# Optimization experiments

Hardware: AMD Instinct MI355X
Metric: run time of the kernel (lower is better)

## Reference

```python
import jax, jax.numpy as jnp
import numpy as np

B, S, D, H, M = 2, 2048, 1024, 16, 4096  # batch, seqlen, dim, n_heads, max_seq_len
HD = D // H  # head_dim = 64
EPS = 1e-5


def layernorm(x, g, b):
    mu = jnp.mean(x, axis=-1, keepdims=True)
    var = jnp.mean((x - mu) ** 2, axis=-1, keepdims=True)
    return (x - mu) * jax.lax.rsqrt(var + EPS) * g + b


def setup_inputs() -> dict:
    key = jax.random.key(0)
    ks = jax.random.split(key, 5)
    x = jax.random.normal(ks[0], (B, S, D), jnp.float32)
    # causal mask: >=0 -> keep, negative -> drop (forward does att *= mask >= 0)
    i = jnp.arange(S)
    mask = jnp.where(i[None, :] <= i[:, None], 0, -1).astype(jnp.int32)[None, None]
    w1 = jax.random.normal(ks[1], (4 * D, D), jnp.float32) * (D ** -0.5)
    b1 = jnp.zeros((4 * D,), jnp.float32)
    w2 = jax.random.normal(ks[2], (D, D), jnp.float32) * (D ** -0.5)
    b2 = jnp.zeros((D,), jnp.float32)
    g1 = jnp.ones((D,), jnp.float32)
    beta1 = jnp.zeros((D,), jnp.float32)
    g2 = jnp.ones((D,), jnp.float32)
    beta2 = jnp.zeros((D,), jnp.float32)
    pos_w = jax.random.normal(ks[3], (2 * M - 1,), jnp.float32) * 0.02
    return dict(x=x, mask=mask, w1=w1, b1=b1, w2=w2, b2=b2,
                g1=g1, beta1=beta1, g2=g2, beta2=beta2, pos_w=pos_w)


def reference(x, mask, w1, b1, w2, b2, g1, beta1, g2, beta2, pos_w):
    # f1 + silu, split into gate u and q/k/v
    h = jax.nn.silu(x @ w1.T + b1)                      # [B,S,4D]
    u, q, k, v = jnp.split(h, 4, axis=-1)
    to_heads = lambda t: t.reshape(B, S, H, HD).transpose(0, 2, 1, 3)  # [B,H,S,HD]
    u, q, k, v = map(to_heads, (u, q, k, v))
    # relative positional bias: bias[i,j] = pos_w[M-1 + (j - i)]
    rel = jnp.arange(S)[None, :] - jnp.arange(S)[:, None]
    bias = pos_w[M - 1 + rel]                           # [S,S]
    att = jax.nn.silu(jnp.einsum('bhqd,bhkd->bhqk', q, k) + bias)
    att = att * (mask >= 0)                             # [B,H,S,S]
    y = jnp.einsum('bhqk,bhkd->bhqd', att, v) * u
    y = y.transpose(0, 2, 1, 3).reshape(B, S, D)
    y = layernorm(y, g1, beta1)
    y = y @ w2.T + b2
    return layernorm(y + x, g2, beta2)
```

## Files before the change

### kernel.cpp

```cpp
#include <hip/hip_runtime.h>
#include <hip/hip_bf16.h>

#define BN   2
#define SEQ  2048
#define DIM  1024
#define NH   16
#define HD   64
#define D4   4096
#define MAXS 4096

using bf16 = __hip_bfloat16;
typedef __bf16 bf16x8 __attribute__((ext_vector_type(8)));
typedef float  f32x4  __attribute__((ext_vector_type(4)));

__device__ __forceinline__ float bf2f(bf16 v){ return __bfloat162float(v); }
__device__ __forceinline__ bf16  f2bf(float v){ return __float2bfloat16(v); }
__device__ __forceinline__ float silu_f(float v){
  const float e = __expf(-v);
  return v * __builtin_amdgcn_rcpf(1.f + e);
}

__device__ __forceinline__ void async16(void* lds, const void* g){
  __builtin_amdgcn_global_load_lds((const __attribute__((address_space(1))) void*)g,
                                   (__attribute__((address_space(3))) void*)lds, 16, 0, 0);
}
__device__ __forceinline__ f32x4 mfma16(bf16x8 a, bf16x8 b, f32x4 c){
  return __builtin_amdgcn_mfma_f32_16x16x32_bf16(a, b, c, 0, 0, 0);
}

__global__ __launch_bounds__(256) void f2bk3(
    const float* __restrict__ a, bf16* __restrict__ ao, int na,
    const float* __restrict__ b, bf16* __restrict__ bo, int nb,
    const float* __restrict__ c, bf16* __restrict__ co)
{
  int i = (blockIdx.x * 256 + threadIdx.x) * 4;
  const float* in; bf16* out;
  if (i < na){ in = a; out = ao; }
  else if (i < na + nb){ in = b; out = bo; i -= na; }
  else { in = c; out = co; i -= na + nb; }
  const float4 v = *(const float4*)(in + i);
  bf16 t0 = f2bf(v.x), t1 = f2bf(v.y), t2 = f2bf(v.z), t3 = f2bf(v.w);
  ushort4 o;
  o.x = *(unsigned short*)&t0; o.y = *(unsigned short*)&t1;
  o.z = *(unsigned short*)&t2; o.w = *(unsigned short*)&t3;
  *(ushort4*)((unsigned short*)out + i) = o;
}

template<int NTOT>
__global__ __launch_bounds__(256) void gemm_bt(
    const bf16* __restrict__ A, const bf16* __restrict__ W,
    const float* __restrict__ bias, bf16* __restrict__ outb, bf16* __restrict__ vt)
{
  constexpr int K = DIM;
  const int ntiles = NTOT / 128;
  const int m0 = (int)(blockIdx.x / ntiles) * 128;
  const int n0 = (int)(blockIdx.x % ntiles) * 128;
  __shared__ bf16 Al[128*32];
  __shared__ bf16 Bl[128*32];
  const int tid = threadIdx.x, wave = tid>>6, lane = tid&63;
  const int quad = lane>>4, l16 = lane&15;
  const int srow = lane>>2;
  const int sg   = ((lane&3) ^ ((lane>>3)&3)) * 8;
  const int wm = (wave>>1)*64, wn = (wave&1)*64;
  const int rkey = ((l16>>1)&3);

  f32x4 acc[4][4];
  #pragma unroll
  for (int i=0;i<4;i++)
    #pragma unroll
    for (int j=0;j<4;j++) acc[i][j] = (f32x4){0.f,0.f,0.f,0.f};

  const bf16* aB = A + m0*K;
  const bf16* wB = W + n0*K;

  for (int k0 = 0; k0 < K; k0 += 32){
    async16(&Al[wave*1024      ], aB + (wave*32      + srow)*K + k0 + sg);
    async16(&Al[wave*1024 + 512], aB + (wave*32 + 16 + srow)*K + k0 + sg);
    async16(&Bl[wave*1024      ], wB + (wave*32      + srow)*K + k0 + sg);
    async16(&Bl[wave*1024 + 512], wB + (wave*32 + 16 + srow)*K + k0 + sg);
    __syncthreads();
    bf16x8 af[4], bv[4];
    #pragma unroll
    for (int mt=0;mt<4;mt++) af[mt] = *(const bf16x8*)&Al[(wm+mt*16+l16)*32 + (quad ^ rkey)*8];
    #pragma unroll
    for (int nt=0;nt<4;nt++) bv[nt] = *(const bf16x8*)&Bl[(wn+nt*16+l16)*32 + (quad ^ rkey)*8];
    #pragma unroll
    for (int mt=0;mt<4;mt++)
      #pragma unroll
      for (int nt=0;nt<4;nt++)
        acc[mt][nt] = mfma16(af[mt], bv[nt], acc[mt][nt]);
    __syncthreads();
  }

  const bool vtile = (NTOT == 4096) && (n0 >= 3*DIM);
  if (!vtile){
    #pragma unroll
    for (int mt=0;mt<4;mt++){
      #pragma unroll
      for (int nt=0;nt<4;nt++){
        const int row = m0 + wm + mt*16 + quad*4;
        const int col = n0 + wn + nt*16 + l16;
        const float bvv = bias[col];
        #pragma unroll
        for (int r=0;r<4;r++){
          float v = silu_f(acc[mt][nt][r] + bvv);
          outb[(row+r)*NTOT + col] = f2bf(v);
        }
      }
    }
  } else {
    #pragma unroll
    for (int mt=0;mt<4;mt++){
      #pragma unroll
      for (int nt=0;nt<4;nt++){
        const int row = m0 + wm + mt*16 + quad*4;
        const int colg = n0 + wn + nt*16 + l16;
        const float bvv = bias[colg];
        const int col = colg - 3*DIM;
        const int hh = col >> 6, d = col & 63;
        const int bb = row >> 11, sl = row & 2047;
        ushort4 o;
        float v0 = silu_f(acc[mt][nt][0] + bvv);
        float v1 = silu_f(acc[mt][nt][1] + bvv);
        float v2 = silu_f(acc[mt][nt][2] + bvv);
        float v3 = silu_f(acc[mt][nt][3] + bvv);
        bf16 t0=f2bf(v0), t1=f2bf(v1), t2=f2bf(v2), t3=f2bf(v3);
        o.x=*(unsigned short*)&t0; o.y=*(unsigned short*)&t1;
        o.z=*(unsigned short*)&t2; o.w=*(unsigned short*)&t3;
        *(ushort4*)&vt[((bb*NH + hh)*HD + d)*SEQ + sl] = o;
      }
    }
  }
}

__global__ __launch_bounds__(256) void gemm_bt2(
    const bf16* __restrict__ A, const bf16* __restrict__ W,
    const float* __restrict__ bias, const float* __restrict__ resid,
    float* __restrict__ outf)
{
  constexpr int K = DIM, NTOT = DIM;
  const int ntiles = NTOT / 64;
  const int m0 = (int)(blockIdx.x / ntiles) * 128;
  const int n0 = (int)(blockIdx.x % ntiles) * 64;
  __shared__ bf16 Al[128*32];
  __shared__ bf16 Bl[64*32];
  const int tid = threadIdx.x, wave = tid>>6, lane = tid&63;
  const int quad = lane>>4, l16 = lane&15;
  const int srow = lane>>2;
  const int sg   = ((lane&3) ^ ((lane>>3)&3)) * 8;
  const int wm = wave*32;
  const int rkey = ((l16>>1)&3);

  f32x4 acc[2][4];
  #pragma unroll
  for (int i=0;i<2;i++)
    #pragma unroll
    for (int j=0;j<4;j++) acc[i][j] = (f32x4){0.f,0.f,0.f,0.f};

  const bf16* aB = A + m0*K;
  const bf16* wB = W + n0*K;

  for (int k0 = 0; k0 < K; k0 += 32){
    async16(&Al[wave*1024      ], aB + (wave*32      + srow)*K + k0 + sg);
    async16(&Al[wave*1024 + 512], aB + (wave*32 + 16 + srow)*K + k0 + sg);
    async16(&Bl[wave*512       ], wB + (wave*16      + srow)*K + k0 + sg);
    __syncthreads();
    bf16x8 af[2], bv[4];
    #pragma unroll
    for (int mt=0;mt<2;mt++) af[mt] = *(const bf16x8*)&Al[(wm+mt*16+l16)*32 + (quad ^ rkey)*8];
    #pragma unroll
    for (int nt=0;nt<4;nt++) bv[nt] = *(const bf16x8*)&Bl[(nt*16+l16)*32 + (quad ^ rkey)*8];
    #pragma unroll
    for (int mt=0;mt<2;mt++)
      #pragma unroll
      for (int nt=0;nt<4;nt++)
        acc[mt][nt] = mfma16(af[mt], bv[nt], acc[mt][nt]);
    __syncthreads();
  }

  #pragma unroll
  for (int mt=0;mt<2;mt++){
    #pragma unroll
    for (int nt=0;nt<4;nt++){
      const int row = m0 + wm + mt*16 + quad*4;
      const int col = n0 + nt*16 + l16;
      const float bvv = bias[col];
      #pragma unroll
      for (int r=0;r<4;r++){
        outf[(row+r)*NTOT + col] = acc[mt][nt][r] + bvv + resid[(row+r)*NTOT + col];
      }
    }
  }
}

__global__ __launch_bounds__(256) void attn(
    const bf16* __restrict__ h, const bf16* __restrict__ vt,
    const float* __restrict__ pw, bf16* __restrict__ y)
{
  const int bid = blockIdx.x;
  const int g  = (bid & 7) + ((bid >> 7) << 3);
  const int qp = (bid >> 3) & 15;
  const int hh = g & 15, b = g >> 4;
  __shared__ bf16 Kl[128*64];
  __shared__ bf16 Vl[64*128];
  __shared__ bf16 Pl[4][16*136];
  __shared__ float pwl[256];
  const int tid = threadIdx.x, wave = tid>>6, lane = tid&63;
  const int quad = lane>>4, l16 = lane&15;

  const bf16* kgb = h + b*SEQ*D4 + 2*DIM + hh*HD;
  const bf16* vgb = vt + (b*NH + hh)*HD*SEQ;
  const int krow8 = lane>>3;
  const int kgo   = ((lane&7) ^ krow8) * 8;
  const int vrow4 = lane>>4;

  #pragma unroll
  for (int pass = 0; pass < 2; ++pass){
    const int qt = pass ? (31 - qp) : qp;
    const int q0 = qt * 64;

    const bf16* qbase = h + (b*SEQ + q0 + wave*16 + l16)*D4 + DIM + hh*HD;
    bf16x8 qf[2];
    qf[0] = *(const bf16x8*)(qbase + quad*8);
    qf[1] = *(const bf16x8*)(qbase + 32 + quad*8);

    f32x4 oacc[4];
    #pragma unroll
    for (int nt=0;nt<4;nt++) oacc[nt] = (f32x4){0.f,0.f,0.f,0.f};

    const int kmax = q0 + 64;
    for (int k0 = 0; k0 < kmax; k0 += 128){
      #pragma unroll
      for (int t=0;t<4;t++)
        async16(&Kl[(wave*32 + t*8)*64], kgb + (k0 + wave*32 + t*8 + krow8)*D4 + kgo);
      #pragma unroll
      for (int t=0;t<4;t++){
        const int vg = ((lane&15) ^ (t*4 + vrow4)) * 8;
        async16(&Vl[(wave*16 + t*4)*128], vgb + (wave*16 + t*4 + vrow4)*SEQ + k0 + vg);
      }
      const int W0 = MAXS - 1 + k0 - q0 - 63;
      pwl[tid] = pw[W0 + tid];
      __syncthreads();

      f32x4 sacc[8];
      #pragma unroll
      for (int nt=0;nt<8;nt++) sacc[nt] = (f32x4){0.f,0.f,0.f,0.f};
      #pragma unroll
      for (int ks=0;ks<2;ks++){
        #pragma unroll
        for (int nt=0;nt<8;nt++){
          bf16x8 kf = *(const bf16x8*)&Kl[(nt*16 + l16)*64 + ((ks*4 + quad) ^ (l16&7))*8];
          sacc[nt] = mfma16(kf, qf[ks], sacc[nt]);
        }
      }

      const int dq = q0 - k0;
      const int qrl = wave*16 + l16;
      #pragma unroll
      for (int nt=0;nt<8;nt++){
        const int kb = nt*16 + quad*4;
        const int d0 = kb - qrl;
        ushort4 o;
        bf16 tb[4];
        #pragma unroll
        for (int r=0;r<4;r++){
          const int d = kb + r - qrl;
          const float bias = pwl[d + 63];
          const float sv = silu_f(sacc[nt][r] + bias);
          tb[r] = f2bf((d <= dq) ? sv : 0.f);
        }
        (void)d0;
        o.x=*(unsigned short*)&tb[0]; o.y=*(unsigned short*)&tb[1];
        o.z=*(unsigned short*)&tb[2]; o.w=*(unsigned short*)&tb[3];
        *(ushort4*)&Pl[wave][l16*136 + kb] = o;
      }

      #pragma unroll
      for (int ks=0;ks<4;ks++){
        bf16x8 pf = *(const bf16x8*)&Pl[wave][l16*136 + ks*32 + quad*8];
        #pragma unroll
        for (int nt=0;nt<4;nt++){
          bf16x8 vf = *(const bf16x8*)&Vl[(nt*16 + l16)*128 + ((ks*4 + quad) ^ l16)*8];
          oacc[nt] = mfma16(pf, vf, oacc[nt]);
        }
      }
      __syncthreads();
    }

    const int qrow = q0 + wave*16 + quad*4;
    #pragma unroll
    for (int nt=0;nt<4;nt++){
      const int c = hh*HD + nt*16 + l16;
      #pragma unroll
      for (int r=0;r<4;r++){
        const int srow = b*SEQ + qrow + r;
        const float uu = bf2f(h[srow*D4 + c]);
        y[srow*DIM + c] = f2bf(oacc[nt][r] * uu);
      }
    }
    __syncthreads();
  }
}


template<bool FP32IN, bool FP32OUT>
__global__ __launch_bounds__(256) void lnorm(const void* __restrict__ in,
    const float* __restrict__ g, const float* __restrict__ be, void* __restrict__ out)
{
  const int row = blockIdx.x;
  const int tid = threadIdx.x, wave = tid>>6, lane = tid&63;
  const int c0 = tid*4;
  float v[4];
  if (FP32IN){
    const float* p = (const float*)in + row*DIM + c0;
    #pragma unroll
    for (int j=0;j<4;j++) v[j] = p[j];
  } else {
    const bf16* p = (const bf16*)in + row*DIM + c0;
    #pragma unroll
    for (int j=0;j<4;j++) v[j] = bf2f(p[j]);
  }
  float s = 0.f, ss = 0.f;
  #pragma unroll
  for (int j=0;j<4;j++){ s += v[j]; ss += v[j]*v[j]; }
  #pragma unroll
  for (int off=32; off>0; off>>=1){
    s  += __shfl_down(s, off);
    ss += __shfl_down(ss, off);
  }
  __shared__ float red[8];
  if (lane==0){ red[wave] = s; red[4+wave] = ss; }
  __syncthreads();
  s  = red[0]+red[1]+red[2]+red[3];
  ss = red[4]+red[5]+red[6]+red[7];
  const float mu   = s * (1.f/DIM);
  const float var  = ss * (1.f/DIM) - mu*mu;
  const float rstd = rsqrtf(var + 1e-5f);
  #pragma unroll
  for (int j=0;j<4;j++){
    const int c = c0 + j;
    const float o = (v[j]-mu)*rstd*g[c] + be[c];
    if (FP32OUT) ((float*)out)[row*DIM + c] = o;
    else         ((bf16*)out)[row*DIM + c] = f2bf(o);
  }
}

extern "C" void kernel_launch(void* const* d_in, const int* in_sizes, int n_in,
                              void* d_out, int out_size, void* d_ws, size_t ws_size,
                              hipStream_t stream)
{
  const float* x   = (const float*)d_in[0];
  const float* w1  = (const float*)d_in[2];
  const float* b1  = (const float*)d_in[3];
  const float* w2  = (const float*)d_in[4];
  const float* b2  = (const float*)d_in[5];
  const float* g1  = (const float*)d_in[6];
  const float* be1 = (const float*)d_in[7];
  const float* g2  = (const float*)d_in[8];
  const float* be2 = (const float*)d_in[9];
  const float* pw  = (const float*)d_in[10];

  char* ws = (char*)d_ws;
  bf16*  h   = (bf16*)(ws);
  bf16*  vt  = (bf16*)(ws + (32u<<20));
  bf16*  y   = (bf16*)(ws + (40u<<20));
  bf16*  xb  = (bf16*)(ws + (48u<<20));
  bf16*  w1b = (bf16*)(ws + (56u<<20));
  bf16*  w2b = (bf16*)(ws + (64u<<20));
  bf16*  l1  = (bf16*)(ws + (66u<<20));
  float* z   = (float*)(ws + (74u<<20));

  const int NX  = BN*SEQ*DIM;
  const int NW1 = 4*DIM*DIM;
  const int NW2 = DIM*DIM;
  f2bk3<<<dim3((NX+NW1+NW2)/1024), dim3(256), 0, stream>>>(x, xb, NX, w1, w1b, NW1, w2, w2b);

  gemm_bt<4096><<<dim3(1024), dim3(256), 0, stream>>>(xb, w1b, b1, h, vt);
  attn<<<dim3(512), dim3(256), 0, stream>>>(h, vt, pw, y);
  lnorm<false,false><<<dim3(4096), dim3(256), 0, stream>>>(y, g1, be1, l1);
  gemm_bt2<<<dim3(512), dim3(256), 0, stream>>>(l1, w2b, b2, x, z);
  lnorm<true,true><<<dim3(4096), dim3(256), 0, stream>>>(z, g2, be2, d_out);
}
```

Measured before the change: 243.0 us.

## Prefetch next K/V tile into registers and raise MFMA wave priority

Replaces the direct global-to-LDS async loads with register prefetching: the next K, V and positional-bias tile is loaded into registers while the current tile's MFMAs run, then stored to LDS at the top of the next iteration. Barrier placement moves so a single sync precedes the LDS store and another follows it. s_setprio is raised around the MFMA blocks to favor matrix issue. This aims to hide global load latency behind compute, at the cost of more registers and extra LDS store instructions.

Measured after the change: 241.7 us. About the same (-0.5%).

```diff
diff --git a/kernel.cpp b/kernel.cpp
--- a/kernel.cpp
+++ b/kernel.cpp
@@ -229,22 +229,47 @@
     for (int nt=0;nt<4;nt++) oacc[nt] = (f32x4){0.f,0.f,0.f,0.f};
 
     const int kmax = q0 + 64;
+
+    bf16x8 kreg[4], vreg[4];
+    float pv;
+    #pragma unroll
+    for (int t=0;t<4;t++)
+      kreg[t] = *(const bf16x8*)(kgb + (wave*32 + t*8 + krow8)*D4 + kgo);
+    #pragma unroll
+    for (int t=0;t<4;t++){
+      const int vg = ((lane&15) ^ (t*4 + vrow4)) * 8;
+      vreg[t] = *(const bf16x8*)(vgb + (wave*16 + t*4 + vrow4)*SEQ + vg);
+    }
+    pv = pw[MAXS - 1 - q0 - 63 + tid];
+
     for (int k0 = 0; k0 < kmax; k0 += 128){
+      __syncthreads();
       #pragma unroll
       for (int t=0;t<4;t++)
-        async16(&Kl[(wave*32 + t*8)*64], kgb + (k0 + wave*32 + t*8 + krow8)*D4 + kgo);
-      #pragma unroll
-      for (int t=0;t<4;t++){
-        const int vg = ((lane&15) ^ (t*4 + vrow4)) * 8;
-        async16(&Vl[(wave*16 + t*4)*128], vgb + (wave*16 + t*4 + vrow4)*SEQ + k0 + vg);
-      }
-      const int W0 = MAXS - 1 + k0 - q0 - 63;
-      pwl[tid] = pw[W0 + tid];
+        *(bf16x8*)&Kl[(wave*32 + t*8)*64 + lane*8] = kreg[t];
+      #pragma unroll
+      for (int t=0;t<4;t++)
+        *(bf16x8*)&Vl[(wave*16 + t*4)*128 + lane*8] = vreg[t];
+      pwl[tid] = pv;
       __syncthreads();
 
+      if (k0 + 128 < kmax){
+        const int kn = k0 + 128;
+        #pragma unroll
+        for (int t=0;t<4;t++)
+          kreg[t] = *(const bf16x8*)(kgb + (kn + wave*32 + t*8 + krow8)*D4 + kgo);
+        #pragma unroll
+        for (int t=0;t<4;t++){
+          const int vg = ((lane&15) ^ (t*4 + vrow4)) * 8;
+          vreg[t] = *(const bf16x8*)(vgb + (wave*16 + t*4 + vrow4)*SEQ + kn + vg);
+        }
+        pv = pw[MAXS - 1 + kn - q0 - 63 + tid];
+      }
+
       f32x4 sacc[8];
       #pragma unroll
       for (int nt=0;nt<8;nt++) sacc[nt] = (f32x4){0.f,0.f,0.f,0.f};
+      __builtin_amdgcn_s_setprio(1);
       #pragma unroll
       for (int ks=0;ks<2;ks++){
         #pragma unroll
@@ -253,13 +278,13 @@
           sacc[nt] = mfma16(kf, qf[ks], sacc[nt]);
         }
       }
+      __builtin_amdgcn_s_setprio(0);
 
       const int dq = q0 - k0;
       const int qrl = wave*16 + l16;
       #pragma unroll
       for (int nt=0;nt<8;nt++){
         const int kb = nt*16 + quad*4;
-        const int d0 = kb - qrl;
         ushort4 o;
         bf16 tb[4];
         #pragma unroll
@@ -269,12 +294,12 @@
           const float sv = silu_f(sacc[nt][r] + bias);
           tb[r] = f2bf((d <= dq) ? sv : 0.f);
         }
-        (void)d0;
         o.x=*(unsigned short*)&tb[0]; o.y=*(unsigned short*)&tb[1];
         o.z=*(unsigned short*)&tb[2]; o.w=*(unsigned short*)&tb[3];
         *(ushort4*)&Pl[wave][l16*136 + kb] = o;
       }
 
+      __builtin_amdgcn_s_setprio(1);
       #pragma unroll
       for (int ks=0;ks<4;ks++){
         bf16x8 pf = *(const bf16x8*)&Pl[wave][l16*136 + ks*32 + quad*8];
@@ -284,7 +309,7 @@
           oacc[nt] = mfma16(pf, vf, oacc[nt]);
         }
       }
-      __syncthreads();
+      __builtin_amdgcn_s_setprio(0);
     }
 
     const int qrow = q0 + wave*16 + quad*4;
```
